# Performance work log

Hardware: AMD Instinct MI355X
Metric: run time of the kernel (lower is better)

## Reference

```python
import jax, jax.numpy as jnp
import numpy as np

N, E = 20000, 100000
IN_CH, HID_CH, EDGE_DIM, NUM_CLASSES = 32, 32, 16, 10


def setup_inputs() -> dict:
    key = jax.random.key(0)
    ks = jax.random.split(key, 20)
    s = 0.05
    inp = {
        "x": jax.random.normal(ks[0], (N, IN_CH), jnp.float32),
        "edge_index": jax.random.randint(ks[1], (2, E), 0, N, jnp.int64),
        "edge_attr": jax.random.normal(ks[2], (E, EDGE_DIM), jnp.float32),
        # edge MLP 1: edge_dim -> in*hid -> in*hid (weights stored as (in, out))
        "e1_w1": jax.random.normal(ks[3], (EDGE_DIM, IN_CH * HID_CH), jnp.float32) * s,
        "e1_b1": jnp.zeros((IN_CH * HID_CH,), jnp.float32),
        "e1_w2": jax.random.normal(ks[4], (IN_CH * HID_CH, IN_CH * HID_CH), jnp.float32) * s,
        "e1_b2": jnp.zeros((IN_CH * HID_CH,), jnp.float32),
        "root1": jax.random.normal(ks[5], (IN_CH, HID_CH), jnp.float32) * s,
        "bias1": jnp.zeros((HID_CH,), jnp.float32),
        # edge MLP 2: edge_dim -> hid*hid -> hid*hid
        "e2_w1": jax.random.normal(ks[6], (EDGE_DIM, HID_CH * HID_CH), jnp.float32) * s,
        "e2_b1": jnp.zeros((HID_CH * HID_CH,), jnp.float32),
        "e2_w2": jax.random.normal(ks[7], (HID_CH * HID_CH, HID_CH * HID_CH), jnp.float32) * s,
        "e2_b2": jnp.zeros((HID_CH * HID_CH,), jnp.float32),
        "root2": jax.random.normal(ks[8], (HID_CH, HID_CH), jnp.float32) * s,
        "bias2": jnp.zeros((HID_CH,), jnp.float32),
        "lin_w": jax.random.normal(ks[9], (HID_CH, NUM_CLASSES), jnp.float32) * s,
        "lin_b": jnp.zeros((NUM_CLASSES,), jnp.float32),
    }
    return inp


def _nnconv_mean(x, src, dst, edge_attr, w1, b1, w2, b2, root, bias, in_ch, out_ch, n_nodes):
    # edge MLP -> per-edge weight matrix [E, in_ch, out_ch]
    h = jax.nn.relu(edge_attr @ w1 + b1) @ w2 + b2
    W = h.reshape(-1, in_ch, out_ch)
    # message: x_j @ W_e (gather source features, per-edge matmul)
    msg = jnp.einsum('ei,eio->eo', x[src], W)
    # scatter-mean to target nodes
    agg = jax.ops.segment_sum(msg, dst, num_segments=n_nodes)
    cnt = jax.ops.segment_sum(jnp.ones((msg.shape[0],), msg.dtype), dst, num_segments=n_nodes)
    mean = agg / jnp.maximum(cnt, 1.0)[:, None]
    return mean + x @ root + bias


def reference(x, edge_index, edge_attr,
              e1_w1, e1_b1, e1_w2, e1_b2, root1, bias1,
              e2_w1, e2_b1, e2_w2, e2_b2, root2, bias2,
              lin_w, lin_b):
    src, dst = edge_index[0], edge_index[1]
    n = x.shape[0]
    h = jax.nn.relu(_nnconv_mean(x, src, dst, edge_attr, e1_w1, e1_b1, e1_w2, e1_b2,
                                 root1, bias1, IN_CH, HID_CH, n))
    # dropout p=0.5 is identity in eval mode
    h = jax.nn.relu(_nnconv_mean(h, src, dst, edge_attr, e2_w1, e2_b1, e2_w2, e2_b2,
                                 root2, bias2, HID_CH, HID_CH, n))
    return h @ lin_w + lin_b
```

## Files before the change

### kernel.cpp

```cpp
#include <hip/hip_runtime.h>

typedef __attribute__((ext_vector_type(8))) short sh8;
typedef __attribute__((ext_vector_type(4))) float f32x4;

#define E_EDGES 100000
#define E_PAD   100096
#define N_NODES 20000

#define BAR() do { __builtin_amdgcn_sched_barrier(0); __builtin_amdgcn_s_barrier(); __builtin_amdgcn_sched_barrier(0); } while (0)
#define WAITV0()    asm volatile("s_waitcnt vmcnt(0)" ::: "memory")
#define WAITLGKM0() asm volatile("s_waitcnt lgkmcnt(0)" ::: "memory")

__device__ __forceinline__ unsigned short f2bf(float f) {
  union { float f; unsigned int u; } v; v.f = f;
  unsigned int r = v.u + 0x7FFFu + ((v.u >> 16) & 1u);
  return (unsigned short)(r >> 16);
}

__device__ __forceinline__ void async16(const void* g, void* l) {
  __builtin_amdgcn_global_load_lds((const __attribute__((address_space(1))) unsigned int*)g,
                                   (__attribute__((address_space(3))) unsigned int*)l,
                                   16, 0, 0);
}

__global__ void transpose_w2_kernel(const float* __restrict__ w2, unsigned short* __restrict__ w2t) {
  __shared__ float tile[32][33];
  int b = blockIdx.x;
  int bx = b & 31, by = b >> 5;
  int lx = threadIdx.x & 31, ly = threadIdx.x >> 5;
#pragma unroll
  for (int j = 0; j < 4; ++j)
    tile[ly + j*8][lx] = w2[(by*32 + ly + j*8)*1024 + bx*32 + lx];
  __syncthreads();
#pragma unroll
  for (int j = 0; j < 4; ++j)
    w2t[(size_t)(bx*32 + ly + j*8)*1024 + by*32 + lx] = f2bf(tile[lx][ly + j*8]);
}

__global__ __launch_bounds__(256)
void edge_mlp1_kernel(const float* __restrict__ ea, const float* __restrict__ w1,
                      const float* __restrict__ b1, unsigned short* __restrict__ h1) {
  __shared__ float eas[8][16];
  const int tid = threadIdx.x;
  const int e0 = blockIdx.x * 8;
  if (tid < 128) {
    int g = tid >> 4, d = tid & 15;
    int ge = e0 + g;
    eas[g][d] = (ge < E_EDGES) ? ea[(size_t)ge*16 + d] : 0.f;
  }
  __syncthreads();
  const int c0 = tid * 4;
  float4 bb = *(const float4*)(b1 + c0);
  float4 acc[8];
#pragma unroll
  for (int g = 0; g < 8; ++g) acc[g] = bb;
#pragma unroll
  for (int d = 0; d < 16; ++d) {
    float4 w = *(const float4*)(w1 + (size_t)d*1024 + c0);
#pragma unroll
    for (int g = 0; g < 8; ++g) {
      float ev = eas[g][d];
      acc[g].x += ev*w.x; acc[g].y += ev*w.y; acc[g].z += ev*w.z; acc[g].w += ev*w.w;
    }
  }
#pragma unroll
  for (int g = 0; g < 8; ++g) {
    ushort4 o;
    if (e0 + g < E_EDGES) {
      o.x = f2bf(fmaxf(acc[g].x, 0.f)); o.y = f2bf(fmaxf(acc[g].y, 0.f));
      o.z = f2bf(fmaxf(acc[g].z, 0.f)); o.w = f2bf(fmaxf(acc[g].w, 0.f));
    } else {
      o.x = o.y = o.z = o.w = 0;
    }
    *(ushort4*)(h1 + (size_t)(e0 + g)*1024 + c0) = o;
  }
}

__global__ void count_kernel(const int* __restrict__ dst, float* __restrict__ cnt) {
  int t = blockIdx.x*256 + threadIdx.x;
  if (t < E_EDGES) atomicAdd(&cnt[dst[t]], 1.0f);
}

__global__ __launch_bounds__(512, 2)
void gemm_scatter_kernel(const unsigned short* __restrict__ h1,
                         const unsigned short* __restrict__ w2t,
                         const float* __restrict__ b2,
                         const float* __restrict__ xin,
                         const int* __restrict__ src,
                         const int* __restrict__ dst,
                         float* __restrict__ agg) {
  __shared__ __align__(16) unsigned short Als[2][256*64];
  __shared__ __align__(16) unsigned short Bls[2][256*64];
  float* msgA = (float*)&Als[0][0];
  float* msgB = (float*)&Bls[0][0];
  float (*xg)[8] = (float (*)[8])((char*)&Als[0][0] + 36864);
  int* dsts = (int*)((char*)&Bls[0][0] + 36864);

  const int tid  = threadIdx.x;
  const int wave = tid >> 6, lane = tid & 63;
  const int wm = wave >> 2, wn = wave & 3;
  const int lr = lane >> 4, lc = lane & 15;

  const int bid = blockIdx.x;
  const int xcd = bid & 7, idx = bid >> 3;
  const int logical = (xcd < 4 ? xcd*196 : 784 + (xcd - 4)*195) + idx;
  const int tile_m = logical >> 2, tile_n = logical & 3;
  const int e0 = tile_m*256, n0 = tile_n*256;

  const unsigned short* Ag = h1  + (size_t)e0*1024;
  const unsigned short* Bg = w2t + (size_t)n0*1024;

  const int rj     = lane >> 3;
  const int colswz = 8*((lane & 7) ^ rj);
  const int swzb   = (lc & 7) << 4;

#define STAGE(buf, kt) do {                                                         \
    _Pragma("unroll")                                                               \
    for (int j = 0; j < 4; ++j) {                                                   \
      int row = (wave*4 + j)*8 + rj;                                                \
      async16(Ag + (size_t)row*1024 + (kt)*64 + colswz, &Als[buf][(wave*4 + j)*512]); \
      async16(Bg + (size_t)row*1024 + (kt)*64 + colswz, &Bls[buf][(wave*4 + j)*512]); \
    }                                                                               \
  } while (0)

  f32x4 acc[8][4];
#pragma unroll
  for (int m = 0; m < 8; ++m)
#pragma unroll
    for (int n = 0; n < 4; ++n) acc[m][n] = (f32x4){0.f, 0.f, 0.f, 0.f};

  STAGE(0, 0);

#pragma unroll
  for (int kt = 0; kt < 16; ++kt) {
    const int cur = kt & 1;
    WAITV0();
    BAR();
    const char* Ab = (const char*)&Als[cur][0];
    const char* Bb = (const char*)&Bls[cur][0];
    sh8 b[4][2], a[8][2];
#pragma unroll
    for (int n = 0; n < 4; ++n)
#pragma unroll
      for (int kk = 0; kk < 2; ++kk)
        b[n][kk] = *(const sh8*)(Bb + (wn*64 + n*16 + lc)*128 + ((kk*64 + lr*16) ^ swzb));
#pragma unroll
    for (int m = 0; m < 8; ++m)
#pragma unroll
      for (int kk = 0; kk < 2; ++kk)
        a[m][kk] = *(const sh8*)(Ab + (wm*128 + m*16 + lc)*128 + ((kk*64 + lr*16) ^ swzb));
    WAITLGKM0();
    BAR();
    if (kt < 15) STAGE(cur ^ 1, kt + 1);
    __builtin_amdgcn_s_setprio(1);
#pragma unroll
    for (int m = 0; m < 8; ++m)
#pragma unroll
      for (int n = 0; n < 4; ++n) {
        acc[m][n] = __builtin_amdgcn_mfma_f32_16x16x32_bf16(a[m][0], b[n][0], acc[m][n], 0, 0, 0);
        acc[m][n] = __builtin_amdgcn_mfma_f32_16x16x32_bf16(a[m][1], b[n][1], acc[m][n], 0, 0, 0);
      }
    __builtin_amdgcn_s_setprio(0);
  }
#undef STAGE

  {
    int e = tid >> 1, half = tid & 1;
    int ge = e0 + e;
    float4 v = make_float4(0.f, 0.f, 0.f, 0.f);
    if (ge < E_EDGES) v = *(const float4*)(xin + (size_t)src[ge]*32 + tile_n*8 + half*4);
    *(float4*)&xg[e][half*4] = v;
    if (tid < 256) dsts[tid] = (e0 + tid < E_EDGES) ? dst[e0 + tid] : -1;
  }
  float b2c[4];
#pragma unroll
  for (int n = 0; n < 4; ++n) b2c[n] = b2[n0 + wn*64 + n*16 + lc];
  WAITLGKM0();
  BAR();

  if ((wn & 1) == 0) {
    float* mb = (wn == 0) ? msgA : msgB;
#pragma unroll
    for (int m = 0; m < 8; ++m)
#pragma unroll
      for (int r = 0; r < 4; ++r) {
        int e = wm*128 + m*16 + lr*4 + r;
        float x0 = xg[e][2*wn], x1 = xg[e][2*wn + 1];
        mb[e*33 + lc]      = (acc[m][0][r] + b2c[0])*x0 + (acc[m][2][r] + b2c[2])*x1;
        mb[e*33 + lc + 16] = (acc[m][1][r] + b2c[1])*x0 + (acc[m][3][r] + b2c[3])*x1;
      }
  }
  BAR();
  if ((wn & 1) == 1) {
    float* mb = (wn == 1) ? msgA : msgB;
#pragma unroll
    for (int m = 0; m < 8; ++m)
#pragma unroll
      for (int r = 0; r < 4; ++r) {
        int e = wm*128 + m*16 + lr*4 + r;
        float x0 = xg[e][2*wn], x1 = xg[e][2*wn + 1];
        mb[e*33 + lc]      += (acc[m][0][r] + b2c[0])*x0 + (acc[m][2][r] + b2c[2])*x1;
        mb[e*33 + lc + 16] += (acc[m][1][r] + b2c[1])*x0 + (acc[m][3][r] + b2c[3])*x1;
      }
  }
  BAR();
  for (int t = tid; t < 256*32; t += 512) {
    int e = t >> 5, o = t & 31;
    int dn = dsts[e];
    if (dn >= 0) atomicAdd(&agg[(size_t)dn*32 + o], msgA[e*33 + o] + msgB[e*33 + o]);
  }
}

__global__ void node_update_kernel(const float* __restrict__ agg, const float* __restrict__ cnt,
                                   const float* __restrict__ xin, const float* __restrict__ root,
                                   const float* __restrict__ bias, float* __restrict__ outp) {
  int t = blockIdx.x*256 + threadIdx.x;
  if (t >= N_NODES*32) return;
  int n = t >> 5, i = t & 31;
  const float* xr = xin + (size_t)n*32;
  float s = bias[i];
#pragma unroll
  for (int j = 0; j < 32; ++j) s += xr[j]*root[j*32 + i];
  float c = cnt[n]; c = c > 1.f ? c : 1.f;
  float v = agg[t]/c + s;
  outp[t] = fmaxf(v, 0.f);
}

__global__ void final_linear_kernel(const float* __restrict__ h, const float* __restrict__ lw,
                                    const float* __restrict__ lb, float* __restrict__ out) {
  int t = blockIdx.x*256 + threadIdx.x;
  if (t >= N_NODES*10) return;
  int n = t / 10, k = t % 10;
  const float* hr = h + (size_t)n*32;
  float s = lb[k];
#pragma unroll
  for (int i = 0; i < 32; ++i) s += hr[i]*lw[i*10 + k];
  out[t] = s;
}

extern "C" void kernel_launch(void* const* d_in, const int* in_sizes, int n_in,
                              void* d_out, int out_size, void* d_ws, size_t ws_size,
                              hipStream_t stream) {
  const float* x     = (const float*)d_in[0];
  const int*   ei    = (const int*)d_in[1];
  const float* ea    = (const float*)d_in[2];
  const float* e1w1  = (const float*)d_in[3];
  const float* e1b1  = (const float*)d_in[4];
  const float* e1w2  = (const float*)d_in[5];
  const float* e1b2  = (const float*)d_in[6];
  const float* root1 = (const float*)d_in[7];
  const float* bias1 = (const float*)d_in[8];
  const float* e2w1  = (const float*)d_in[9];
  const float* e2b1  = (const float*)d_in[10];
  const float* e2w2  = (const float*)d_in[11];
  const float* e2b2  = (const float*)d_in[12];
  const float* root2 = (const float*)d_in[13];
  const float* bias2 = (const float*)d_in[14];
  const float* linw  = (const float*)d_in[15];
  const float* linb  = (const float*)d_in[16];
  const int* srcp = ei;
  const int* dstp = ei + E_EDGES;

  char* ws = (char*)d_ws;
  size_t off = 0;
  auto alloc = [&](size_t bytes) { void* p = ws + off; off += (bytes + 255) & ~(size_t)255; return p; };
  unsigned short* h1buf = (unsigned short*)alloc((size_t)E_PAD*1024*2);
  unsigned short* w2t   = (unsigned short*)alloc((size_t)1024*1024*2);
  float* agg  = (float*)alloc((size_t)N_NODES*32*4);
  float* cnt  = (float*)alloc((size_t)N_NODES*4);
  float* out1 = (float*)alloc((size_t)N_NODES*32*4);
  float* hbuf = (float*)alloc((size_t)N_NODES*32*4);
  (void)ws_size; (void)n_in; (void)in_sizes; (void)out_size;

  hipMemsetAsync(agg, 0, (size_t)N_NODES*32*4, stream);
  hipMemsetAsync(cnt, 0, (size_t)N_NODES*4, stream);
  count_kernel<<<(E_EDGES + 255)/256, 256, 0, stream>>>(dstp, cnt);

  const int gemm_grid = (E_PAD/256) * 4;

  transpose_w2_kernel<<<1024, 256, 0, stream>>>(e1w2, w2t);
  edge_mlp1_kernel<<<E_PAD/8, 256, 0, stream>>>(ea, e1w1, e1b1, h1buf);
  gemm_scatter_kernel<<<gemm_grid, 512, 0, stream>>>(h1buf, w2t, e1b2, x, srcp, dstp, agg);
  node_update_kernel<<<(N_NODES*32 + 255)/256, 256, 0, stream>>>(agg, cnt, x, root1, bias1, out1);

  hipMemsetAsync(agg, 0, (size_t)N_NODES*32*4, stream);
  transpose_w2_kernel<<<1024, 256, 0, stream>>>(e2w2, w2t);
  edge_mlp1_kernel<<<E_PAD/8, 256, 0, stream>>>(ea, e2w1, e2b1, h1buf);
  gemm_scatter_kernel<<<gemm_grid, 512, 0, stream>>>(h1buf, w2t, e2b2, out1, srcp, dstp, agg);
  node_update_kernel<<<(N_NODES*32 + 255)/256, 256, 0, stream>>>(agg, cnt, out1, root2, bias2, hbuf);

  final_linear_kernel<<<(N_NODES*10 + 255)/256, 256, 0, stream>>>(hbuf, linw, linb, (float*)d_out);
}
```

Before: 780.1 us.

## Triple-buffer A tiles and drop the second per-iteration barrier in GEMM-scatter

The main GEMM loop moves from a shared double buffer for A and B to one 160 KB LDS array: A gets three buffers with prefetch two k-steps ahead, and B stays double-buffered. Loads are now issued right after the single barrier, and a partial `vmcnt(4)` wait replaces the full drain. This removes the second barrier and the `lgkmcnt(0)` wait from each iteration and keeps more global loads in flight, so memory latency overlaps better with the MFMAs. In exchange the block uses more LDS, which limits residency to one block per CU and leaves no spare LDS, and the epilogue gets explicit `__syncthreads` calls.

```diff
diff --git a/kernel.cpp b/kernel.cpp
--- a/kernel.cpp
+++ b/kernel.cpp
@@ -8,8 +8,6 @@
 #define N_NODES 20000
 
 #define BAR() do { __builtin_amdgcn_sched_barrier(0); __builtin_amdgcn_s_barrier(); __builtin_amdgcn_sched_barrier(0); } while (0)
-#define WAITV0()    asm volatile("s_waitcnt vmcnt(0)" ::: "memory")
-#define WAITLGKM0() asm volatile("s_waitcnt lgkmcnt(0)" ::: "memory")
 
 __device__ __forceinline__ unsigned short f2bf(float f) {
   union { float f; unsigned int u; } v; v.f = f;
@@ -89,12 +87,11 @@
                          const int* __restrict__ src,
                          const int* __restrict__ dst,
                          float* __restrict__ agg) {
-  __shared__ __align__(16) unsigned short Als[2][256*64];
-  __shared__ __align__(16) unsigned short Bls[2][256*64];
-  float* msgA = (float*)&Als[0][0];
-  float* msgB = (float*)&Bls[0][0];
-  float (*xg)[8] = (float (*)[8])((char*)&Als[0][0] + 36864);
-  int* dsts = (int*)((char*)&Bls[0][0] + 36864);
+  __shared__ __align__(16) unsigned char lds[163840];
+  float* msgA = (float*)lds;
+  float* msgB = (float*)(lds + 33792);
+  float (*xg)[8] = (float (*)[8])(lds + 67584);
+  int* dsts = (int*)(lds + 75776);
 
   const int tid  = threadIdx.x;
   const int wave = tid >> 6, lane = tid & 63;
@@ -105,23 +102,26 @@
   const int xcd = bid & 7, idx = bid >> 3;
   const int logical = (xcd < 4 ? xcd*196 : 784 + (xcd - 4)*195) + idx;
   const int tile_m = logical >> 2, tile_n = logical & 3;
-  const int e0 = tile_m*256, n0 = tile_n*256;
+  const long e0 = (long)tile_m * 256, n0 = (long)tile_n * 256;
 
   const unsigned short* Ag = h1  + (size_t)e0*1024;
   const unsigned short* Bg = w2t + (size_t)n0*1024;
 
-  const int rj     = lane >> 3;
-  const int colswz = 8*((lane & 7) ^ rj);
-  const int swzb   = (lc & 7) << 4;
-
-#define STAGE(buf, kt) do {                                                         \
-    _Pragma("unroll")                                                               \
-    for (int j = 0; j < 4; ++j) {                                                   \
-      int row = (wave*4 + j)*8 + rj;                                                \
-      async16(Ag + (size_t)row*1024 + (kt)*64 + colswz, &Als[buf][(wave*4 + j)*512]); \
-      async16(Bg + (size_t)row*1024 + (kt)*64 + colswz, &Bls[buf][(wave*4 + j)*512]); \
-    }                                                                               \
-  } while (0)
+  const int l8   = lane >> 3;
+  const int scol = 8*((lane & 7) ^ l8);
+  const int srow = wave*8 + l8;
+  const int swzb = (lc & 7) << 4;
+
+#define ABUF(i) (lds + (i)*32768)
+#define BBUF(i) (lds + 98304 + (i)*32768)
+#define STAGE_A(bi, kt) do { _Pragma("unroll")                                      \
+    for (int j = 0; j < 4; ++j)                                                     \
+      async16(Ag + (size_t)(srow + 64*j)*1024 + (kt)*64 + scol,                     \
+              ABUF(bi) + (wave*8 + 64*j)*128); } while (0)
+#define STAGE_B(bi, kt) do { _Pragma("unroll")                                      \
+    for (int j = 0; j < 4; ++j)                                                     \
+      async16(Bg + (size_t)(srow + 64*j)*1024 + (kt)*64 + scol,                     \
+              BBUF(bi) + (wave*8 + 64*j)*128); } while (0)
 
   f32x4 acc[8][4];
 #pragma unroll
@@ -129,16 +129,20 @@
 #pragma unroll
     for (int n = 0; n < 4; ++n) acc[m][n] = (f32x4){0.f, 0.f, 0.f, 0.f};
 
-  STAGE(0, 0);
+  STAGE_B(0, 0);
+  STAGE_A(0, 0);
+  STAGE_A(1, 1);
 
 #pragma unroll
   for (int kt = 0; kt < 16; ++kt) {
-    const int cur = kt & 1;
-    WAITV0();
+    if (kt == 15) asm volatile("s_waitcnt vmcnt(0)" ::: "memory");
+    else          asm volatile("s_waitcnt vmcnt(4)" ::: "memory");
     BAR();
-    const char* Ab = (const char*)&Als[cur][0];
-    const char* Bb = (const char*)&Bls[cur][0];
-    sh8 b[4][2], a[8][2];
+    if (kt + 1 < 16) STAGE_B((kt + 1) & 1, kt + 1);
+    if (kt + 2 < 16) STAGE_A((kt + 2) % 3, kt + 2);
+    const char* Ab = (const char*)ABUF(kt % 3);
+    const char* Bb = (const char*)BBUF(kt & 1);
+    sh8 a[8][2], b[4][2];
 #pragma unroll
     for (int n = 0; n < 4; ++n)
 #pragma unroll
@@ -149,9 +153,6 @@
 #pragma unroll
       for (int kk = 0; kk < 2; ++kk)
         a[m][kk] = *(const sh8*)(Ab + (wm*128 + m*16 + lc)*128 + ((kk*64 + lr*16) ^ swzb));
-    WAITLGKM0();
-    BAR();
-    if (kt < 15) STAGE(cur ^ 1, kt + 1);
     __builtin_amdgcn_s_setprio(1);
 #pragma unroll
     for (int m = 0; m < 8; ++m)
@@ -162,11 +163,15 @@
       }
     __builtin_amdgcn_s_setprio(0);
   }
-#undef STAGE
-
+#undef STAGE_A
+#undef STAGE_B
+#undef ABUF
+#undef BBUF
+
+  __syncthreads();
   {
     int e = tid >> 1, half = tid & 1;
-    int ge = e0 + e;
+    long ge = e0 + e;
     float4 v = make_float4(0.f, 0.f, 0.f, 0.f);
     if (ge < E_EDGES) v = *(const float4*)(xin + (size_t)src[ge]*32 + tile_n*8 + half*4);
     *(float4*)&xg[e][half*4] = v;
@@ -175,8 +180,7 @@
   float b2c[4];
 #pragma unroll
   for (int n = 0; n < 4; ++n) b2c[n] = b2[n0 + wn*64 + n*16 + lc];
-  WAITLGKM0();
-  BAR();
+  __syncthreads();
 
   if ((wn & 1) == 0) {
     float* mb = (wn == 0) ? msgA : msgB;
@@ -190,7 +194,7 @@
         mb[e*33 + lc + 16] = (acc[m][1][r] + b2c[1])*x0 + (acc[m][3][r] + b2c[3])*x1;
       }
   }
-  BAR();
+  __syncthreads();
   if ((wn & 1) == 1) {
     float* mb = (wn == 1) ? msgA : msgB;
 #pragma unroll
@@ -203,7 +207,7 @@
         mb[e*33 + lc + 16] += (acc[m][1][r] + b2c[1])*x0 + (acc[m][3][r] + b2c[3])*x1;
       }
   }
-  BAR();
+  __syncthreads();
   for (int t = tid; t < 256*32; t += 512) {
     int e = t >> 5, o = t & 31;
     int dn = dsts[e];
```

After: 980.9 us. 1.26x slower.
